# Performance work log

Hardware: AMD Instinct MI355X
Metric: run time of the kernel (lower is better)

The kernel has to match this reference:

```python
import jax, jax.numpy as jnp
import numpy as np

EMBED, HEADS, LEVELS, POINTS, CAMS, ZANCH = 256, 8, 4, 8, 6, 4
HEAD_DIM = EMBED // HEADS
NQ, BS = 10000, 1
SHAPES = np.array([[92, 160], [46, 80], [23, 40], [12, 20]], dtype=np.int64)
NV = int((SHAPES[:, 0] * SHAPES[:, 1]).sum())  # 19560


def setup_inputs() -> dict:
    key = jax.random.key(0)
    ks = jax.random.split(key, 10)
    f = lambda k, s, sc=1.0: jax.random.normal(k, s, dtype=jnp.float32) * sc
    lsi = np.concatenate([[0], np.cumsum(SHAPES[:, 0] * SHAPES[:, 1])[:-1]]).astype(np.int64)
    return dict(
        query=f(ks[0], (BS, NQ, EMBED)),
        query_pos=f(ks[1], (BS, NQ, EMBED)),
        value=f(ks[2], (CAMS, NV, BS, EMBED)),
        reference_points=jax.random.uniform(ks[3], (CAMS, BS, NQ, ZANCH, 2), dtype=jnp.float32),
        bev_mask=jax.random.bernoulli(ks[4], 0.3, (CAMS, BS, NQ, ZANCH)),
        spatial_shapes=jnp.asarray(SHAPES),
        level_start_index=jnp.asarray(lsi),
        Wv=f(ks[5], (EMBED, EMBED), 0.02), bv=jnp.zeros((EMBED,), jnp.float32),
        Woff=f(ks[6], (EMBED, HEADS * LEVELS * POINTS * 2), 0.02),
        boff=f(ks[7], (HEADS * LEVELS * POINTS * 2,), 0.5),
        Watt=f(ks[8], (EMBED, HEADS * LEVELS * POINTS), 0.02),
        batt=jnp.zeros((HEADS * LEVELS * POINTS,), jnp.float32),
        Wout=f(ks[9], (EMBED, EMBED), 0.02), bout=jnp.zeros((EMBED,), jnp.float32),
    )


def _bilinear_gather(v2, x, y, H, W):
    # v2: (BH, H*W, hd); x, y: (BH, N) pixel coords. grid_sample bilinear,
    # align_corners=False, padding_mode='zeros' semantics.
    x0 = jnp.floor(x); y0 = jnp.floor(y)
    lx = x - x0; ly = y - y0
    x0i = x0.astype(jnp.int32); y0i = y0.astype(jnp.int32)
    out = jnp.zeros(x.shape + (v2.shape[-1],), v2.dtype)
    for dx, dy, w in ((0, 0, (1 - lx) * (1 - ly)), (1, 0, lx * (1 - ly)),
                      (0, 1, (1 - lx) * ly), (1, 1, lx * ly)):
        xi = x0i + dx; yi = y0i + dy
        valid = (xi >= 0) & (xi < W) & (yi >= 0) & (yi < H)
        idx = jnp.clip(yi, 0, H - 1) * W + jnp.clip(xi, 0, W - 1)
        g = jnp.take_along_axis(v2, idx[..., None], axis=1)
        out = out + g * (w * valid.astype(v2.dtype))[..., None]
    return out


def _ms_deform_attn(q, v, ref, shapes, lsi, Wv, bv, Woff, boff, Watt, batt):
    # q: (B, nq, C); v: (B, nv, C); ref: (B, nq, D, 2)
    B, nq, C = q.shape
    v = (v @ Wv + bv).reshape(B, -1, HEADS, HEAD_DIM)
    off = (q @ Woff + boff).reshape(B, nq, HEADS, LEVELS, POINTS, 2)
    attw = jax.nn.softmax((q @ Watt + batt).reshape(B, nq, HEADS, LEVELS * POINTS), axis=-1)
    attw = attw.reshape(B, nq, HEADS, LEVELS, POINTS)
    # offset normalizer: (w_l, h_l) per level
    norm = jnp.asarray(np.stack([shapes[:, 1], shapes[:, 0]], -1), q.dtype)  # (L, 2)
    off = off / norm[None, None, None, :, None, :]
    off = off.reshape(B, nq, HEADS, LEVELS, POINTS // ZANCH, ZANCH, 2)
    loc = (ref[:, :, None, None, None] + off).reshape(B, nq, HEADS, LEVELS, POINTS, 2)
    acc = jnp.zeros((B, HEADS, nq, HEAD_DIM), q.dtype)
    for l in range(LEVELS):
        H, W = int(shapes[l, 0]), int(shapes[l, 1])
        s = int(lsi[l])
        vl = v[:, s:s + H * W].transpose(0, 2, 1, 3).reshape(B * HEADS, H * W, HEAD_DIM)
        ll = loc[:, :, :, l].transpose(0, 2, 1, 3, 4).reshape(B * HEADS, nq * POINTS, 2)
        x = ll[..., 0] * W - 0.5
        y = ll[..., 1] * H - 0.5
        samp = _bilinear_gather(vl, x, y, H, W).reshape(B, HEADS, nq, POINTS, HEAD_DIM)
        w = attw[:, :, :, l].transpose(0, 2, 1, 3)  # (B, HEADS, nq, POINTS)
        acc = acc + (samp * w[..., None]).sum(3)
    return acc.transpose(0, 2, 1, 3).reshape(B, nq, C)


def reference(query, query_pos, value, reference_points, bev_mask, spatial_shapes,
              level_start_index, Wv, bv, Woff, boff, Watt, batt, Wout, bout):
    shapes = np.asarray(spatial_shapes)
    lsi = np.asarray(level_start_index)
    B, nq, C = query.shape
    cams = value.shape[0]
    q = query + query_pos
    # replicate queries per camera (equivalent to rebatch-by-mask: unselected
    # outputs are masked out before accumulation)
    q_cam = jnp.broadcast_to(q[:, None], (B, cams, nq, C)).reshape(B * cams, nq, C)
    v = value.transpose(2, 0, 1, 3).reshape(B * cams, -1, C)
    ref = reference_points.transpose(1, 0, 2, 3, 4).reshape(B * cams, nq, ZANCH, 2)
    out = _ms_deform_attn(q_cam, v, ref, shapes, lsi, Wv, bv, Woff, boff, Watt, batt)
    out = out.reshape(B, cams, nq, C)
    # query selection per camera uses batch 0 of bev_mask, as in the original
    m = (bev_mask[:, 0].sum(-1) > 0)  # (cams, nq)
    slots = (out * m[None, :, :, None].astype(out.dtype)).sum(1)  # (B, nq, C)
    count = (bev_mask.sum(-1) > 0).astype(query.dtype).transpose(1, 2, 0).sum(-1)
    count = jnp.maximum(count, 1.0)  # (B, nq)
    slots = slots / count[..., None]
    # dropout in eval mode is identity
    return slots @ Wout + bout + query
```

## Files before the change

kernel.cpp:

```cpp
#include <hip/hip_runtime.h>
#include <hip/hip_bf16.h>

constexpr int NQ = 10000, NV = 19560, CAMS = 6, EMBED = 256, HEADS = 8,
              HEAD_DIM = 32, LEVELS = 4, POINTS = 8;
constexpr int MQ_PAD = 10112;
constexpr int MV_PAD = 117376;
constexpr int NBUCK = CAMS * 128;
constexpr int MAXITEMS = CAMS * NQ * 4;

typedef unsigned int u32;
typedef unsigned short u16;
typedef unsigned char u8;
typedef __attribute__((ext_vector_type(8))) short short8v;
typedef __attribute__((ext_vector_type(4))) float f32x4;
typedef __attribute__((ext_vector_type(2))) float f32x2;

__device__ inline u16 f2bf(float f) {
  __hip_bfloat16 b = __float2bfloat16(f);
  return *(u16*)&b;
}
__device__ inline float bf2f(u16 v) { union { u32 i; float f; } x; x.i = (u32)v << 16; return x.f; }

__global__ void conv_bf16_kernel(const float* __restrict__ a, const float* __restrict__ b,
                                 u16* __restrict__ dst, int M, int Mpad) {
  int i = blockIdx.x * blockDim.x + threadIdx.x;
  if (i >= Mpad * 32) return;
  int row = i >> 5;
  int col = (i & 31) * 8;
  u16 o[8];
  if (row < M) {
    const float* pa = a + (size_t)row * 256 + col;
#pragma unroll
    for (int j = 0; j < 8; ++j) {
      float v = pa[j];
      if (b) v += b[(size_t)row * 256 + col + j];
      o[j] = f2bf(v);
    }
  } else {
#pragma unroll
    for (int j = 0; j < 8; ++j) o[j] = 0;
  }
  *(short8v*)&dst[(size_t)row * 256 + col] = *(short8v*)o;
}

__global__ void transpose_w_kernel(const float* __restrict__ src, u16* __restrict__ dst, int N) {
  int g = blockIdx.x * blockDim.x + threadIdx.x;
  if (g >= N * 256) return;
  int n = g >> 8, k = g & 255;
  dst[(size_t)n * 256 + k] = f2bf(src[(size_t)k * N + n]);
}

__device__ inline int orig_off_col(int j) {
  int z = (j >> 7) & 3, h = (j >> 4) & 7, l = (j >> 2) & 3, pi = (j >> 1) & 1, xy = j & 1;
  return h * 64 + l * 16 + (z + 4 * pi) * 2 + xy;
}
__device__ inline int orig_att_col(int j) {
  int z = (j >> 6) & 3, h = (j >> 3) & 7, l = (j >> 1) & 3, pi = j & 1;
  return h * 32 + l * 8 + (z + 4 * pi);
}
__global__ void transpose_wq_kernel(const float* __restrict__ Woff, const float* __restrict__ Watt,
                                    const float* __restrict__ boff, const float* __restrict__ batt,
                                    u16* __restrict__ WqT, float* __restrict__ catb) {
  int g = blockIdx.x * blockDim.x + threadIdx.x;
  if (g >= 768 * 256) return;
  int j = g >> 8, k = g & 255;
  float v;
  if (j < 512) v = Woff[(size_t)k * 512 + orig_off_col(j)];
  else         v = Watt[(size_t)k * 256 + orig_att_col(j - 512)];
  WqT[(size_t)j * 256 + k] = f2bf(v);
  if (k == 0) catb[j] = (j < 512) ? boff[orig_off_col(j)] : batt[orig_att_col(j - 512)];
}

__device__ inline int buck_key(int c, float rx, float ry) {
  int tx = min(max((int)(rx * 16.f), 0), 15);
  int ty = min(max((int)(ry * 8.f), 0), 7);
  return c * 128 + ty * 16 + tx;
}

__global__ void mask_kernel(const int* __restrict__ bev, const float* __restrict__ ref,
                            unsigned char* __restrict__ m, float* __restrict__ cinv,
                            u32* __restrict__ hist) {
  int q = blockIdx.x * blockDim.x + threadIdx.x;
  if (q >= NQ) return;
  int cnt = 0;
  for (int c = 0; c < CAMS; ++c) {
    int any = 0;
    for (int z = 0; z < 4; ++z) any |= bev[((size_t)c * NQ + q) * 4 + z];
    m[c * NQ + q] = (unsigned char)(any != 0);
    cnt += (any != 0);
    if (any) {
      const float* rc = ref + ((size_t)c * NQ + q) * 8;
#pragma unroll
      for (int z = 0; z < 4; ++z)
        atomicAdd(&hist[buck_key(c, rc[z * 2], rc[z * 2 + 1])], 1u);
    }
  }
  cinv[q] = 1.0f / (float)(cnt > 0 ? cnt : 1);
}

__global__ void scan_kernel(const u32* __restrict__ hist, u32* __restrict__ cursor,
                            u32* __restrict__ total) {
  __shared__ u32 tmp[NBUCK];
  int t = threadIdx.x;
  u32 v = hist[t];
  tmp[t] = v;
  __syncthreads();
  for (int d = 1; d < NBUCK; d <<= 1) {
    u32 add = (t >= d) ? tmp[t - d] : 0;
    __syncthreads();
    tmp[t] += add;
    __syncthreads();
  }
  cursor[t] = tmp[t] - v;
  if (t == NBUCK - 1) *total = tmp[t];
}

__global__ void scatter_kernel(const float* __restrict__ ref, const unsigned char* __restrict__ m,
                               u32* __restrict__ cursor, u32* __restrict__ perm) {
  int q = blockIdx.x * blockDim.x + threadIdx.x;
  if (q >= NQ) return;
  for (int c = 0; c < CAMS; ++c) {
    if (!m[c * NQ + q]) continue;
    const float* rc = ref + ((size_t)c * NQ + q) * 8;
#pragma unroll
    for (int z = 0; z < 4; ++z) {
      u32 pos = atomicAdd(&cursor[buck_key(c, rc[z * 2], rc[z * 2 + 1])], 1u);
      perm[pos] = ((u32)c << 16) | ((u32)z << 14) | (u32)q;
    }
  }
}

__global__ __launch_bounds__(256) void gemm_mfma(
    const u16* __restrict__ A, const u16* __restrict__ Bt,
    const float* __restrict__ bias, const float* __restrict__ add,
    void* __restrict__ Cout, void* __restrict__ Cout2, int M, int N, int mode) {
  constexpr int K = 256, BK = 64;
  __shared__ u16 As[128 * BK];
  __shared__ u16 Bs[128 * BK];
  const int tid = threadIdx.x;
  const int lane = tid & 63, w = tid >> 6;
  const int wr = w >> 1, wc = w & 1;
  const int row0 = blockIdx.y * 128, col0 = blockIdx.x * 128;
  f32x4 acc[4][4] = {};

  for (int k0 = 0; k0 < K; k0 += BK) {
    short8v areg[4], breg[4];
#pragma unroll
    for (int j = 0; j < 4; ++j) {
      int e = tid + j * 256;
      int r = e >> 3, cb = (e & 7) * 16;
      areg[j] = *(const short8v*)((const char*)A + ((size_t)(row0 + r) * K + k0) * 2 + cb);
      breg[j] = *(const short8v*)((const char*)Bt + ((size_t)(col0 + r) * K + k0) * 2 + cb);
    }
    __syncthreads();
#pragma unroll
    for (int j = 0; j < 4; ++j) {
      int e = tid + j * 256;
      int r = e >> 3, cb = (e & 7) * 16;
      int sw = cb ^ ((r & 7) << 4);
      *(short8v*)((char*)As + r * 128 + sw) = areg[j];
      *(short8v*)((char*)Bs + r * 128 + sw) = breg[j];
    }
    __syncthreads();
#pragma unroll
    for (int kk = 0; kk < 2; ++kk) {
      short8v af[4], bf[4];
#pragma unroll
      for (int m = 0; m < 4; ++m) {
        int r = wr * 64 + m * 16 + (lane & 15);
        int cb = kk * 64 + (lane >> 4) * 16;
        af[m] = *(const short8v*)((const char*)As + r * 128 + (cb ^ ((r & 7) << 4)));
      }
#pragma unroll
      for (int n = 0; n < 4; ++n) {
        int r = wc * 64 + n * 16 + (lane & 15);
        int cb = kk * 64 + (lane >> 4) * 16;
        bf[n] = *(const short8v*)((const char*)Bs + r * 128 + (cb ^ ((r & 7) << 4)));
      }
#pragma unroll
      for (int m = 0; m < 4; ++m)
#pragma unroll
        for (int n = 0; n < 4; ++n)
          acc[m][n] = __builtin_amdgcn_mfma_f32_16x16x32_bf16(af[m], bf[n], acc[m][n], 0, 0, 0);
    }
  }

#pragma unroll
  for (int m = 0; m < 4; ++m) {
    int rowb = row0 + wr * 64 + m * 16 + (lane >> 4) * 4;
#pragma unroll
    for (int r = 0; r < 4; ++r) {
      int rr = rowb + r;
      if (rr >= M) continue;
#pragma unroll
      for (int n = 0; n < 4; ++n) {
        int col = col0 + wc * 64 + n * 16 + (lane & 15);
        float v = acc[m][n][r] + bias[col];
        if (mode == 0) {
          ((float*)Cout)[(size_t)rr * N + col] = v;
        } else if (mode == 2) {
          ((float*)Cout)[(size_t)rr * N + col] = v + add[(size_t)rr * N + col];
        } else {
          if (col < 512) ((float*)Cout)[(size_t)rr * 512 + col] = v;
          else           ((float*)Cout2)[(size_t)rr * 256 + (col - 512)] = v;
        }
      }
    }
  }
}

__global__ __launch_bounds__(512) void gemm_wv_f32(
    const float* __restrict__ A, const u16* __restrict__ Bt,
    const float* __restrict__ bias, u8* __restrict__ Cout, int M) {
  constexpr int K = 256, BK = 64;
  __shared__ u16 As[128 * BK];
  __shared__ u16 Bs[256 * BK];
  const int tid = threadIdx.x;
  const int lane = tid & 63, w = tid >> 6;
  const int wr = w >> 2, wc = w & 3;
  const int row0 = blockIdx.x * 128;
  f32x4 acc[4][4] = {};

  for (int k0 = 0; k0 < K; k0 += BK) {
    short8v areg[2], breg[4];
#pragma unroll
    for (int j = 0; j < 2; ++j) {
      int e = tid + j * 512;
      int r = e >> 3, co = (e & 7) * 8;
      u16 tmp[8];
      if (row0 + r < M) {
        const float* src = A + (size_t)(row0 + r) * K + k0 + co;
        float4 f0 = *(const float4*)src;
        float4 f1 = *(const float4*)(src + 4);
        tmp[0] = f2bf(f0.x); tmp[1] = f2bf(f0.y); tmp[2] = f2bf(f0.z); tmp[3] = f2bf(f0.w);
        tmp[4] = f2bf(f1.x); tmp[5] = f2bf(f1.y); tmp[6] = f2bf(f1.z); tmp[7] = f2bf(f1.w);
      } else {
#pragma unroll
        for (int t = 0; t < 8; ++t) tmp[t] = 0;
      }
      areg[j] = *(short8v*)tmp;
    }
#pragma unroll
    for (int j = 0; j < 4; ++j) {
      int e = tid + j * 512;
      int r = e >> 3, cb = (e & 7) * 16;
      breg[j] = *(const short8v*)((const char*)Bt + ((size_t)r * K + k0) * 2 + cb);
    }
    __syncthreads();
#pragma unroll
    for (int j = 0; j < 2; ++j) {
      int e = tid + j * 512;
      int r = e >> 3, cb = (e & 7) * 16;
      *(short8v*)((char*)As + r * 128 + (cb ^ ((r & 7) << 4))) = areg[j];
    }
#pragma unroll
    for (int j = 0; j < 4; ++j) {
      int e = tid + j * 512;
      int r = e >> 3, cb = (e & 7) * 16;
      *(short8v*)((char*)Bs + r * 128 + (cb ^ ((r & 7) << 4))) = breg[j];
    }
    __syncthreads();
#pragma unroll
    for (int kk = 0; kk < 2; ++kk) {
      short8v af[4], bf[4];
#pragma unroll
      for (int m = 0; m < 4; ++m) {
        int r = wr * 64 + m * 16 + (lane & 15);
        int cb = kk * 64 + (lane >> 4) * 16;
        af[m] = *(const short8v*)((const char*)As + r * 128 + (cb ^ ((r & 7) << 4)));
      }
#pragma unroll
      for (int n = 0; n < 4; ++n) {
        int r = wc * 64 + n * 16 + (lane & 15);
        int cb = kk * 64 + (lane >> 4) * 16;
        bf[n] = *(const short8v*)((const char*)Bs + r * 128 + (cb ^ ((r & 7) << 4)));
      }
#pragma unroll
      for (int m = 0; m < 4; ++m)
#pragma unroll
        for (int n = 0; n < 4; ++n)
          acc[m][n] = __builtin_amdgcn_mfma_f32_16x16x32_bf16(af[m], bf[n], acc[m][n], 0, 0, 0);
    }
  }

#pragma unroll
  for (int m = 0; m < 4; ++m) {
    int rowb = row0 + wr * 64 + m * 16 + (lane >> 4) * 4;
#pragma unroll
    for (int r = 0; r < 4; ++r) {
      int rr = rowb + r;
      if (rr >= M) continue;
      int cam = rr / NV;
      int px = rr - cam * NV;
#pragma unroll
      for (int n = 0; n < 4; ++n) {
        int col = wc * 64 + n * 16 + (lane & 15);
        float v = acc[m][n][r] + bias[col];
        int h = col >> 5, d = col & 31;
        int pk = __builtin_amdgcn_cvt_pk_fp8_f32(v, v, 0, false);
        Cout[(((size_t)cam * HEADS + h) * NV + px) * 32 + d] = (u8)(pk & 0xff);
      }
    }
  }
}

__global__ void softmax_kernel(float* __restrict__ att) {
  int r = blockIdx.x * blockDim.x + threadIdx.x;
  if (r >= NQ * HEADS) return;
  int q = r >> 3, h = r & 7;
  float* base = att + (size_t)q * 256 + h * 8;
  float v[32];
  float mx = -1e30f;
  int n = 0;
#pragma unroll
  for (int z = 0; z < 4; ++z)
#pragma unroll
    for (int l = 0; l < 4; ++l)
#pragma unroll
      for (int pi = 0; pi < 2; ++pi) {
        float x = base[z * 64 + l * 2 + pi];
        v[n++] = x;
        mx = fmaxf(mx, x);
      }
  float sm = 0.f;
#pragma unroll
  for (int i = 0; i < 32; ++i) { v[i] = expf(v[i] - mx); sm += v[i]; }
  float inv = 1.0f / sm;
  n = 0;
#pragma unroll
  for (int z = 0; z < 4; ++z)
#pragma unroll
    for (int l = 0; l < 4; ++l)
#pragma unroll
      for (int pi = 0; pi < 2; ++pi)
        base[z * 64 + l * 2 + pi] = v[n++] * inv;
}

__global__ __launch_bounds__(256, 8) void sample_kernel(
    const u8* __restrict__ vproj, const float* __restrict__ offr,
    const float* __restrict__ attw, const float* __restrict__ ref,
    const u32* __restrict__ perm, const u32* __restrict__ total,
    u16* __restrict__ part2) {
  constexpr int Hs[4] = {92, 46, 23, 12};
  constexpr int Ws[4] = {160, 80, 40, 20};
  constexpr int LSI[4] = {0, 14720, 18400, 19320};
  const int idx = blockIdx.x * 4 + (threadIdx.x >> 6);
  if (idx >= (int)*total) return;
  const u32 item = perm[idx];
  const int c = item >> 16;
  const int z = (item >> 14) & 3;
  const int q = item & 0x3fff;
  const int lane = threadIdx.x & 63;
  const int h = lane >> 3;
  const int pp = (lane >> 2) & 1;
  const int d0 = (lane & 3) * 8;

  const float* rc = ref + ((size_t)c * NQ + q) * 8 + z * 2;
  const float rx = rc[0], ry = rc[1];
  const float* offq = offr + (size_t)q * 512 + z * 128 + h * 16;
  const float* attq = attw + (size_t)q * 256 + z * 64 + h * 8;
  const u8* vch = vproj + ((size_t)c * HEADS + h) * NV * 32 + d0;

  f32x2 acc2[4] = {};
#pragma unroll 2
  for (int l = 0; l < LEVELS; ++l) {
    const int W = Ws[l], H = Hs[l];
    const u8* vl = vch + (size_t)LSI[l] * 32;
    float2 o = *(const float2*)&offq[l * 4 + pp * 2];
    float a = attq[l * 2 + pp];
    float x = rx * (float)W + o.x - 0.5f;
    float y = ry * (float)H + o.y - 0.5f;
    float x0f = floorf(x), y0f = floorf(y);
    float lx = x - x0f, ly = y - y0f;
    int x0 = (int)x0f, y0 = (int)y0f;
    float fx0 = (x0 >= 0 && x0 < W) ? 1.f : 0.f;
    float fx1 = (x0 >= -1 && x0 < W - 1) ? 1.f : 0.f;
    float fy0 = (y0 >= 0 && y0 < H) ? 1.f : 0.f;
    float fy1 = (y0 >= -1 && y0 < H - 1) ? 1.f : 0.f;
    int x0c = min(max(x0, 0), W - 1);
    int x1c = min(max(x0 + 1, 0), W - 1);
    int y0c = min(max(y0, 0), H - 1);
    int y1c = min(max(y0 + 1, 0), H - 1);
    uint2 v00 = *(const uint2*)(vl + (size_t)(y0c * W + x0c) * 32);
    uint2 v01 = *(const uint2*)(vl + (size_t)(y0c * W + x1c) * 32);
    uint2 v10 = *(const uint2*)(vl + (size_t)(y1c * W + x0c) * 32);
    uint2 v11 = *(const uint2*)(vl + (size_t)(y1c * W + x1c) * 32);
    float c00 = a * (1.f - lx) * (1.f - ly) * fx0 * fy0;
    float c01 = a * lx * (1.f - ly) * fx1 * fy0;
    float c10 = a * (1.f - lx) * ly * fx0 * fy1;
    float c11 = a * lx * ly * fx1 * fy1;
#pragma unroll
    for (int half = 0; half < 2; ++half) {
      u32 w00 = half ? v00.y : v00.x, w01 = half ? v01.y : v01.x;
      u32 w10 = half ? v10.y : v10.x, w11 = half ? v11.y : v11.x;
      f32x2 gA0 = __builtin_amdgcn_cvt_pk_f32_fp8(w00, false);
      f32x2 gA1 = __builtin_amdgcn_cvt_pk_f32_fp8(w00, true);
      f32x2 gB0 = __builtin_amdgcn_cvt_pk_f32_fp8(w01, false);
      f32x2 gB1 = __builtin_amdgcn_cvt_pk_f32_fp8(w01, true);
      f32x2 gC0 = __builtin_amdgcn_cvt_pk_f32_fp8(w10, false);
      f32x2 gC1 = __builtin_amdgcn_cvt_pk_f32_fp8(w10, true);
      f32x2 gD0 = __builtin_amdgcn_cvt_pk_f32_fp8(w11, false);
      f32x2 gD1 = __builtin_amdgcn_cvt_pk_f32_fp8(w11, true);
      int b = half * 2;
      acc2[b + 0] += gA0 * c00 + gB0 * c01 + gC0 * c10 + gD0 * c11;
      acc2[b + 1] += gA1 * c00 + gB1 * c01 + gC1 * c10 + gD1 * c11;
    }
  }
  float accs[8] = {acc2[0].x, acc2[0].y, acc2[1].x, acc2[1].y,
                   acc2[2].x, acc2[2].y, acc2[3].x, acc2[3].y};
#pragma unroll
  for (int d = 0; d < 8; ++d) accs[d] += __shfl_xor(accs[d], 4);
  if (pp == 0) {
    u16 o[8];
#pragma unroll
    for (int d = 0; d < 8; ++d) o[d] = f2bf(accs[d]);
    short8v* sp = (short8v*)&part2[((size_t)(z * CAMS + c) * NQ + q) * EMBED + h * 32 + d0];
    __builtin_nontemporal_store(*(short8v*)o, sp);
  }
}

__global__ void reduce_kernel(const u16* __restrict__ part2, const unsigned char* __restrict__ m,
                              const float* __restrict__ cinv, u16* __restrict__ sbf) {
  int i = blockIdx.x * blockDim.x + threadIdx.x;
  if (i >= MQ_PAD * 32) return;
  int row = i >> 5;
  int col = (i & 31) * 8;
  u16 o[8];
  if (row < NQ) {
    float s[8] = {};
    for (int c = 0; c < CAMS; ++c) {
      if (!m[c * NQ + row]) continue;
#pragma unroll
      for (int z = 0; z < 4; ++z) {
        const short8v* pp = (const short8v*)&part2[((size_t)(z * CAMS + c) * NQ + row) * EMBED + col];
        short8v v = __builtin_nontemporal_load(pp);
#pragma unroll
        for (int j = 0; j < 8; ++j) s[j] += bf2f((u16)v[j]);
      }
    }
    float sc = cinv[row];
#pragma unroll
    for (int j = 0; j < 8; ++j) o[j] = f2bf(s[j] * sc);
  } else {
#pragma unroll
    for (int j = 0; j < 8; ++j) o[j] = 0;
  }
  *(short8v*)&sbf[(size_t)row * 256 + col] = *(short8v*)o;
}

extern "C" void kernel_launch(void* const* d_in, const int* in_sizes, int n_in,
                              void* d_out, int out_size, void* d_ws, size_t ws_size,
                              hipStream_t stream) {
  const float* query     = (const float*)d_in[0];
  const float* query_pos = (const float*)d_in[1];
  const float* value     = (const float*)d_in[2];
  const float* refpts    = (const float*)d_in[3];
  const int*   bev       = (const int*)d_in[4];
  const float* Wv   = (const float*)d_in[7];
  const float* bv   = (const float*)d_in[8];
  const float* Woff = (const float*)d_in[9];
  const float* boff = (const float*)d_in[10];
  const float* Watt = (const float*)d_in[11];
  const float* batt = (const float*)d_in[12];
  const float* Wout = (const float*)d_in[13];
  const float* bout = (const float*)d_in[14];
  float* out = (float*)d_out;

  char* ws = (char*)d_ws;
  auto alloc = [&](size_t bytes) {
    char* p = ws;
    ws += (bytes + 255) & ~(size_t)255;
    return p;
  };
  u16*   qbf   = (u16*)alloc((size_t)MQ_PAD * 256 * 2);
  u16*   sbf   = (u16*)alloc((size_t)MQ_PAD * 256 * 2);
  u16*   WvT   = (u16*)alloc((size_t)256 * 256 * 2);
  u16*   WqT   = (u16*)alloc((size_t)768 * 256 * 2);
  u16*   WoutT = (u16*)alloc((size_t)256 * 256 * 2);
  float* catb  = (float*)alloc((size_t)768 * 4);
  float* offr  = (float*)alloc((size_t)MQ_PAD * 512 * 4);
  float* attw  = (float*)alloc((size_t)MQ_PAD * 256 * 4);
  u8*    vproj = (u8*)alloc((size_t)CAMS * NV * EMBED);
  u16*   part2 = (u16*)alloc((size_t)4 * CAMS * NQ * EMBED * 2);
  float* cinv  = (float*)alloc((size_t)NQ * 4);
  unsigned char* msk = (unsigned char*)alloc((size_t)CAMS * NQ);
  u32*   hist  = (u32*)alloc((size_t)NBUCK * 4);
  u32*   cursor= (u32*)alloc((size_t)NBUCK * 4);
  u32*   total = (u32*)alloc(256);
  u32*   perm  = (u32*)alloc((size_t)MAXITEMS * 4);

  hipMemsetAsync(hist, 0, NBUCK * 4, stream);

  conv_bf16_kernel<<<(MQ_PAD * 32 + 255) / 256, 256, 0, stream>>>(query, query_pos, qbf, NQ, MQ_PAD);
  mask_kernel<<<(NQ + 255) / 256, 256, 0, stream>>>(bev, refpts, msk, cinv, hist);
  transpose_wq_kernel<<<(768 * 256 + 255) / 256, 256, 0, stream>>>(Woff, Watt, boff, batt, WqT, catb);
  transpose_w_kernel<<<256, 256, 0, stream>>>(Wv, WvT, 256);
  transpose_w_kernel<<<256, 256, 0, stream>>>(Wout, WoutT, 256);

  scan_kernel<<<1, NBUCK, 0, stream>>>(hist, cursor, total);
  scatter_kernel<<<(NQ + 255) / 256, 256, 0, stream>>>(refpts, msk, cursor, perm);

  dim3 gQ(768 / 128, MQ_PAD / 128);
  gemm_mfma<<<gQ, 256, 0, stream>>>(qbf, WqT, catb, nullptr, offr, attw, NQ, 768, 3);
  softmax_kernel<<<(NQ * HEADS + 255) / 256, 256, 0, stream>>>(attw);

  gemm_wv_f32<<<MV_PAD / 128, 512, 0, stream>>>(value, WvT, bv, vproj, CAMS * NV);

  sample_kernel<<<MAXITEMS / 4, 256, 0, stream>>>(vproj, offr, attw, refpts, perm, total, part2);

  reduce_kernel<<<(MQ_PAD * 32 + 255) / 256, 256, 0, stream>>>(part2, msk, cinv, sbf);
  dim3 gOut(256 / 128, MQ_PAD / 128);
  gemm_mfma<<<gOut, 256, 0, stream>>>(sbf, WoutT, bout, query, out, nullptr, NQ, 256, 2);
}
```

Before: 443.9 us.

## Remap sample lanes to one bilinear sample each with full-channel loads

Each lane of the sampling kernel now handles one (head, level, point) sample and loads all 32 fp8 channels of each bilinear corner with two 16-byte loads. Before, four lanes split the channels and each lane looped over the four levels. All corner loads are now issued up front to raise memory-level parallelism and cut per-sample index math. Partial sums are combined with a three-step cross-lane shuffle reduction before a single lane writes the bf16 row. The per-lane register footprint grows (16 float2 accumulators), so the launch-bounds occupancy hint drops from 8 to 4 blocks, and the reduction adds many more shuffles.

```diff
diff --git a/kernel.cpp b/kernel.cpp
--- a/kernel.cpp
+++ b/kernel.cpp
@@ -336,7 +336,7 @@
         base[z * 64 + l * 2 + pi] = v[n++] * inv;
 }
 
-__global__ __launch_bounds__(256, 8) void sample_kernel(
+__global__ __launch_bounds__(256, 4) void sample_kernel(
     const u8* __restrict__ vproj, const float* __restrict__ offr,
     const float* __restrict__ attw, const float* __restrict__ ref,
     const u32* __restrict__ perm, const u32* __restrict__ total,
@@ -352,70 +352,81 @@
   const int q = item & 0x3fff;
   const int lane = threadIdx.x & 63;
   const int h = lane >> 3;
-  const int pp = (lane >> 2) & 1;
-  const int d0 = (lane & 3) * 8;
-
+  const int l = (lane >> 1) & 3;
+  const int pi = lane & 1;
+
+  const int W = Ws[l], H = Hs[l];
   const float* rc = ref + ((size_t)c * NQ + q) * 8 + z * 2;
   const float rx = rc[0], ry = rc[1];
-  const float* offq = offr + (size_t)q * 512 + z * 128 + h * 16;
-  const float* attq = attw + (size_t)q * 256 + z * 64 + h * 8;
-  const u8* vch = vproj + ((size_t)c * HEADS + h) * NV * 32 + d0;
-
-  f32x2 acc2[4] = {};
-#pragma unroll 2
-  for (int l = 0; l < LEVELS; ++l) {
-    const int W = Ws[l], H = Hs[l];
-    const u8* vl = vch + (size_t)LSI[l] * 32;
-    float2 o = *(const float2*)&offq[l * 4 + pp * 2];
-    float a = attq[l * 2 + pp];
-    float x = rx * (float)W + o.x - 0.5f;
-    float y = ry * (float)H + o.y - 0.5f;
-    float x0f = floorf(x), y0f = floorf(y);
-    float lx = x - x0f, ly = y - y0f;
-    int x0 = (int)x0f, y0 = (int)y0f;
-    float fx0 = (x0 >= 0 && x0 < W) ? 1.f : 0.f;
-    float fx1 = (x0 >= -1 && x0 < W - 1) ? 1.f : 0.f;
-    float fy0 = (y0 >= 0 && y0 < H) ? 1.f : 0.f;
-    float fy1 = (y0 >= -1 && y0 < H - 1) ? 1.f : 0.f;
-    int x0c = min(max(x0, 0), W - 1);
-    int x1c = min(max(x0 + 1, 0), W - 1);
-    int y0c = min(max(y0, 0), H - 1);
-    int y1c = min(max(y0 + 1, 0), H - 1);
-    uint2 v00 = *(const uint2*)(vl + (size_t)(y0c * W + x0c) * 32);
-    uint2 v01 = *(const uint2*)(vl + (size_t)(y0c * W + x1c) * 32);
-    uint2 v10 = *(const uint2*)(vl + (size_t)(y1c * W + x0c) * 32);
-    uint2 v11 = *(const uint2*)(vl + (size_t)(y1c * W + x1c) * 32);
-    float c00 = a * (1.f - lx) * (1.f - ly) * fx0 * fy0;
-    float c01 = a * lx * (1.f - ly) * fx1 * fy0;
-    float c10 = a * (1.f - lx) * ly * fx0 * fy1;
-    float c11 = a * lx * ly * fx1 * fy1;
-#pragma unroll
-    for (int half = 0; half < 2; ++half) {
-      u32 w00 = half ? v00.y : v00.x, w01 = half ? v01.y : v01.x;
-      u32 w10 = half ? v10.y : v10.x, w11 = half ? v11.y : v11.x;
-      f32x2 gA0 = __builtin_amdgcn_cvt_pk_f32_fp8(w00, false);
-      f32x2 gA1 = __builtin_amdgcn_cvt_pk_f32_fp8(w00, true);
-      f32x2 gB0 = __builtin_amdgcn_cvt_pk_f32_fp8(w01, false);
-      f32x2 gB1 = __builtin_amdgcn_cvt_pk_f32_fp8(w01, true);
-      f32x2 gC0 = __builtin_amdgcn_cvt_pk_f32_fp8(w10, false);
-      f32x2 gC1 = __builtin_amdgcn_cvt_pk_f32_fp8(w10, true);
-      f32x2 gD0 = __builtin_amdgcn_cvt_pk_f32_fp8(w11, false);
-      f32x2 gD1 = __builtin_amdgcn_cvt_pk_f32_fp8(w11, true);
-      int b = half * 2;
-      acc2[b + 0] += gA0 * c00 + gB0 * c01 + gC0 * c10 + gD0 * c11;
-      acc2[b + 1] += gA1 * c00 + gB1 * c01 + gC1 * c10 + gD1 * c11;
-    }
-  }
-  float accs[8] = {acc2[0].x, acc2[0].y, acc2[1].x, acc2[1].y,
-                   acc2[2].x, acc2[2].y, acc2[3].x, acc2[3].y};
-#pragma unroll
-  for (int d = 0; d < 8; ++d) accs[d] += __shfl_xor(accs[d], 4);
-  if (pp == 0) {
-    u16 o[8];
-#pragma unroll
-    for (int d = 0; d < 8; ++d) o[d] = f2bf(accs[d]);
-    short8v* sp = (short8v*)&part2[((size_t)(z * CAMS + c) * NQ + q) * EMBED + h * 32 + d0];
-    __builtin_nontemporal_store(*(short8v*)o, sp);
+  float2 o = *(const float2*)&offr[(size_t)q * 512 + z * 128 + h * 16 + l * 4 + pi * 2];
+  float a = attw[(size_t)q * 256 + z * 64 + h * 8 + l * 2 + pi];
+  const u8* vl = vproj + ((size_t)c * HEADS + h) * NV * 32 + (size_t)LSI[l] * 32;
+
+  float x = rx * (float)W + o.x - 0.5f;
+  float y = ry * (float)H + o.y - 0.5f;
+  float x0f = floorf(x), y0f = floorf(y);
+  float lx = x - x0f, ly = y - y0f;
+  int x0 = (int)x0f, y0 = (int)y0f;
+  float fx0 = (x0 >= 0 && x0 < W) ? 1.f : 0.f;
+  float fx1 = (x0 >= -1 && x0 < W - 1) ? 1.f : 0.f;
+  float fy0 = (y0 >= 0 && y0 < H) ? 1.f : 0.f;
+  float fy1 = (y0 >= -1 && y0 < H - 1) ? 1.f : 0.f;
+  int x0c = min(max(x0, 0), W - 1);
+  int x1c = min(max(x0 + 1, 0), W - 1);
+  int y0c = min(max(y0, 0), H - 1);
+  int y1c = min(max(y0 + 1, 0), H - 1);
+  float c00 = a * (1.f - lx) * (1.f - ly) * fx0 * fy0;
+  float c01 = a * lx * (1.f - ly) * fx1 * fy0;
+  float c10 = a * (1.f - lx) * ly * fx0 * fy1;
+  float c11 = a * lx * ly * fx1 * fy1;
+
+  const u8* p00 = vl + (size_t)(y0c * W + x0c) * 32;
+  const u8* p01 = vl + (size_t)(y0c * W + x1c) * 32;
+  const u8* p10 = vl + (size_t)(y1c * W + x0c) * 32;
+  const u8* p11 = vl + (size_t)(y1c * W + x1c) * 32;
+  uint4 A0 = *(const uint4*)p00, A1 = *(const uint4*)(p00 + 16);
+  uint4 B0 = *(const uint4*)p01, B1 = *(const uint4*)(p01 + 16);
+  uint4 C0 = *(const uint4*)p10, C1 = *(const uint4*)(p10 + 16);
+  uint4 D0 = *(const uint4*)p11, D1 = *(const uint4*)(p11 + 16);
+
+  f32x2 acc[16] = {};
+  auto consume = [&](uint4 lo, uint4 hi, float wgt) {
+    const u32 wds[8] = {lo.x, lo.y, lo.z, lo.w, hi.x, hi.y, hi.z, hi.w};
+#pragma unroll
+    for (int j = 0; j < 8; ++j) {
+      f32x2 g0 = __builtin_amdgcn_cvt_pk_f32_fp8(wds[j], false);
+      f32x2 g1 = __builtin_amdgcn_cvt_pk_f32_fp8(wds[j], true);
+      acc[2 * j + 0] += g0 * wgt;
+      acc[2 * j + 1] += g1 * wgt;
+    }
+  };
+  consume(A0, A1, c00);
+  consume(B0, B1, c01);
+  consume(C0, C1, c10);
+  consume(D0, D1, c11);
+
+#pragma unroll
+  for (int mask = 1; mask <= 4; mask <<= 1) {
+#pragma unroll
+    for (int j = 0; j < 16; ++j) {
+      f32x2 t;
+      t.x = __shfl_xor(acc[j].x, mask);
+      t.y = __shfl_xor(acc[j].y, mask);
+      acc[j] += t;
+    }
+  }
+
+  if ((lane & 7) == 0) {
+    u16 o16[32];
+#pragma unroll
+    for (int j = 0; j < 16; ++j) {
+      o16[2 * j + 0] = f2bf(acc[j].x);
+      o16[2 * j + 1] = f2bf(acc[j].y);
+    }
+    u16* row = part2 + ((size_t)(z * CAMS + c) * NQ + q) * EMBED + h * 32;
+#pragma unroll
+    for (int j = 0; j < 4; ++j)
+      __builtin_nontemporal_store(*(short8v*)&o16[j * 8], (short8v*)(row + j * 8));
   }
 }
 
```

Result: slower. 477.8 us (+7.6%).

## Fuse camera/anchor reduction into output projection GEMM A-tile load

Applied to the files above, without the earlier changes.

Removes the separate reduce kernel and its bf16 intermediate buffer. The output GEMM now sums the masked per-camera, per-anchor partials, scales them, and converts to bf16 directly while loading its A tiles. It uses 128x256 tiles with 512 threads, so each block covers all output columns and every partial is read once. The sampling kernel's level loop is also fully unrolled. The trade-off is that the GEMM grid shrinks to about 79 blocks, and the reduction loads sit in the GEMM's critical path without overlap, which may underuse the GPU.

```diff
diff --git a/kernel.cpp b/kernel.cpp
--- a/kernel.cpp
+++ b/kernel.cpp
@@ -198,8 +198,6 @@
         float v = acc[m][n][r] + bias[col];
         if (mode == 0) {
           ((float*)Cout)[(size_t)rr * N + col] = v;
-        } else if (mode == 2) {
-          ((float*)Cout)[(size_t)rr * N + col] = v + add[(size_t)rr * N + col];
         } else {
           if (col < 512) ((float*)Cout)[(size_t)rr * 512 + col] = v;
           else           ((float*)Cout2)[(size_t)rr * 256 + (col - 512)] = v;
@@ -299,6 +297,107 @@
         int h = col >> 5, d = col & 31;
         int pk = __builtin_amdgcn_cvt_pk_fp8_f32(v, v, 0, false);
         Cout[(((size_t)cam * HEADS + h) * NV + px) * 32 + d] = (u8)(pk & 0xff);
+      }
+    }
+  }
+}
+
+__global__ __launch_bounds__(512) void gemm_out_fused(
+    const u16* __restrict__ part2, const unsigned char* __restrict__ msk,
+    const float* __restrict__ cinv, const u16* __restrict__ Bt,
+    const float* __restrict__ bias, const float* __restrict__ add,
+    float* __restrict__ Cout) {
+  constexpr int K = 256, BK = 64, M = NQ;
+  __shared__ u16 As[128 * BK];
+  __shared__ u16 Bs[256 * BK];
+  const int tid = threadIdx.x;
+  const int lane = tid & 63, w = tid >> 6;
+  const int wr = w >> 2, wc = w & 3;
+  const int row0 = blockIdx.x * 128;
+  f32x4 acc[4][4] = {};
+
+  for (int k0 = 0; k0 < K; k0 += BK) {
+    short8v areg[2], breg[4];
+#pragma unroll
+    for (int j = 0; j < 2; ++j) {
+      int e = tid + j * 512;
+      int r = e >> 3, co = (e & 7) * 8;
+      int row = row0 + r;
+      u16 tmp[8];
+      if (row < M) {
+        float s[8] = {};
+        for (int c = 0; c < CAMS; ++c) {
+          if (!msk[c * NQ + row]) continue;
+#pragma unroll
+          for (int z = 0; z < 4; ++z) {
+            short8v v = *(const short8v*)&part2[((size_t)(z * CAMS + c) * NQ + row) * EMBED + k0 + co];
+#pragma unroll
+            for (int t = 0; t < 8; ++t) s[t] += bf2f((u16)v[t]);
+          }
+        }
+        float sc = cinv[row];
+#pragma unroll
+        for (int t = 0; t < 8; ++t) tmp[t] = f2bf(s[t] * sc);
+      } else {
+#pragma unroll
+        for (int t = 0; t < 8; ++t) tmp[t] = 0;
+      }
+      areg[j] = *(short8v*)tmp;
+    }
+#pragma unroll
+    for (int j = 0; j < 4; ++j) {
+      int e = tid + j * 512;
+      int r = e >> 3, cb = (e & 7) * 16;
+      breg[j] = *(const short8v*)((const char*)Bt + ((size_t)r * K + k0) * 2 + cb);
+    }
+    __syncthreads();
+#pragma unroll
+    for (int j = 0; j < 2; ++j) {
+      int e = tid + j * 512;
+      int r = e >> 3, cb = (e & 7) * 16;
+      *(short8v*)((char*)As + r * 128 + (cb ^ ((r & 7) << 4))) = areg[j];
+    }
+#pragma unroll
+    for (int j = 0; j < 4; ++j) {
+      int e = tid + j * 512;
+      int r = e >> 3, cb = (e & 7) * 16;
+      *(short8v*)((char*)Bs + r * 128 + (cb ^ ((r & 7) << 4))) = breg[j];
+    }
+    __syncthreads();
+#pragma unroll
+    for (int kk = 0; kk < 2; ++kk) {
+      short8v af[4], bf[4];
+#pragma unroll
+      for (int m = 0; m < 4; ++m) {
+        int r = wr * 64 + m * 16 + (lane & 15);
+        int cb = kk * 64 + (lane >> 4) * 16;
+        af[m] = *(const short8v*)((const char*)As + r * 128 + (cb ^ ((r & 7) << 4)));
+      }
+#pragma unroll
+      for (int n = 0; n < 4; ++n) {
+        int r = wc * 64 + n * 16 + (lane & 15);
+        int cb = kk * 64 + (lane >> 4) * 16;
+        bf[n] = *(const short8v*)((const char*)Bs + r * 128 + (cb ^ ((r & 7) << 4)));
+      }
+#pragma unroll
+      for (int m = 0; m < 4; ++m)
+#pragma unroll
+        for (int n = 0; n < 4; ++n)
+          acc[m][n] = __builtin_amdgcn_mfma_f32_16x16x32_bf16(af[m], bf[n], acc[m][n], 0, 0, 0);
+    }
+  }
+
+#pragma unroll
+  for (int m = 0; m < 4; ++m) {
+    int rowb = row0 + wr * 64 + m * 16 + (lane >> 4) * 4;
+#pragma unroll
+    for (int r = 0; r < 4; ++r) {
+      int rr = rowb + r;
+      if (rr >= M) continue;
+#pragma unroll
+      for (int n = 0; n < 4; ++n) {
+        int col = wc * 64 + n * 16 + (lane & 15);
+        Cout[(size_t)rr * 256 + col] = acc[m][n][r] + bias[col] + add[(size_t)rr * 256 + col];
       }
     }
   }
@@ -362,7 +461,7 @@
   const u8* vch = vproj + ((size_t)c * HEADS + h) * NV * 32 + d0;
 
   f32x2 acc2[4] = {};
-#pragma unroll 2
+#pragma unroll
   for (int l = 0; l < LEVELS; ++l) {
     const int W = Ws[l], H = Hs[l];
     const u8* vl = vch + (size_t)LSI[l] * 32;
@@ -419,35 +518,6 @@
   }
 }
 
-__global__ void reduce_kernel(const u16* __restrict__ part2, const unsigned char* __restrict__ m,
-                              const float* __restrict__ cinv, u16* __restrict__ sbf) {
-  int i = blockIdx.x * blockDim.x + threadIdx.x;
-  if (i >= MQ_PAD * 32) return;
-  int row = i >> 5;
-  int col = (i & 31) * 8;
-  u16 o[8];
-  if (row < NQ) {
-    float s[8] = {};
-    for (int c = 0; c < CAMS; ++c) {
-      if (!m[c * NQ + row]) continue;
-#pragma unroll
-      for (int z = 0; z < 4; ++z) {
-        const short8v* pp = (const short8v*)&part2[((size_t)(z * CAMS + c) * NQ + row) * EMBED + col];
-        short8v v = __builtin_nontemporal_load(pp);
-#pragma unroll
-        for (int j = 0; j < 8; ++j) s[j] += bf2f((u16)v[j]);
-      }
-    }
-    float sc = cinv[row];
-#pragma unroll
-    for (int j = 0; j < 8; ++j) o[j] = f2bf(s[j] * sc);
-  } else {
-#pragma unroll
-    for (int j = 0; j < 8; ++j) o[j] = 0;
-  }
-  *(short8v*)&sbf[(size_t)row * 256 + col] = *(short8v*)o;
-}
-
 extern "C" void kernel_launch(void* const* d_in, const int* in_sizes, int n_in,
                               void* d_out, int out_size, void* d_ws, size_t ws_size,
                               hipStream_t stream) {
@@ -473,7 +543,6 @@
     return p;
   };
   u16*   qbf   = (u16*)alloc((size_t)MQ_PAD * 256 * 2);
-  u16*   sbf   = (u16*)alloc((size_t)MQ_PAD * 256 * 2);
   u16*   WvT   = (u16*)alloc((size_t)256 * 256 * 2);
   u16*   WqT   = (u16*)alloc((size_t)768 * 256 * 2);
   u16*   WoutT = (u16*)alloc((size_t)256 * 256 * 2);
@@ -508,7 +577,5 @@
 
   sample_kernel<<<MAXITEMS / 4, 256, 0, stream>>>(vproj, offr, attw, refpts, perm, total, part2);
 
-  reduce_kernel<<<(MQ_PAD * 32 + 255) / 256, 256, 0, stream>>>(part2, msk, cinv, sbf);
-  dim3 gOut(256 / 128, MQ_PAD / 128);
-  gemm_mfma<<<gOut, 256, 0, stream>>>(sbf, WoutT, bout, query, out, nullptr, NQ, 256, 2);
-}
+  gemm_out_fused<<<MQ_PAD / 128, 512, 0, stream>>>(part2, msk, cinv, WoutT, bout, query, out);
+}
```

New measurement: 448.7 us. About the same (+1.1%).
